# Kernel optimization log

Hardware: AMD Instinct MI355X
Metric: run time of the kernel (lower is better)

Reference implementation:

```python
import jax, jax.numpy as jnp
import numpy as np

N = 50000       # nodes
E = 800000      # edges (before self-loops)
F_IN = 128
HID = 64
HEADS = 4
OUT_DIM = 128
N_CLS = 2
NG = 500        # num graphs
SLOPE = 0.2     # GATConv leaky_relu negative slope
EPS = 1e-5      # BatchNorm eps


def setup_inputs() -> dict:
    key = jax.random.key(0)
    ks = jax.random.split(key, 24)
    s = 0.05
    d = {
        "x": jax.random.normal(ks[0], (N, F_IN), jnp.float32),
        "edge_index": jax.random.randint(ks[1], (2, E), 0, N, jnp.int64),
        "batch": jnp.sort(jax.random.randint(ks[2], (N,), 0, NG, jnp.int64)),
        # GATConv 1
        "W1": jax.random.normal(ks[3], (F_IN, HEADS * HID), jnp.float32) * s,
        "att_src1": jax.random.normal(ks[4], (HEADS, HID), jnp.float32) * s,
        "att_dst1": jax.random.normal(ks[5], (HEADS, HID), jnp.float32) * s,
        "b1": jnp.zeros((HEADS * HID,), jnp.float32),
        # BN1 (eval mode)
        "g1": jnp.ones((HEADS * HID,), jnp.float32),
        "be1": jnp.zeros((HEADS * HID,), jnp.float32),
        "rm1": jnp.zeros((HEADS * HID,), jnp.float32),
        "rv1": jnp.ones((HEADS * HID,), jnp.float32),
        # GATConv 2
        "W2": jax.random.normal(ks[6], (HEADS * HID, HEADS * HID), jnp.float32) * s,
        "att_src2": jax.random.normal(ks[7], (HEADS, HID), jnp.float32) * s,
        "att_dst2": jax.random.normal(ks[8], (HEADS, HID), jnp.float32) * s,
        "b2": jnp.zeros((HEADS * HID,), jnp.float32),
        # BN2 (eval mode)
        "g2": jnp.ones((HEADS * HID,), jnp.float32),
        "be2": jnp.zeros((HEADS * HID,), jnp.float32),
        "rm2": jnp.zeros((HEADS * HID,), jnp.float32),
        "rv2": jnp.ones((HEADS * HID,), jnp.float32),
        # MLP head
        "lw1": jax.random.normal(ks[9], (HEADS * HID, OUT_DIM), jnp.float32) * s,
        "lb1": jnp.zeros((OUT_DIM,), jnp.float32),
        "lw2": jax.random.normal(ks[10], (OUT_DIM, N_CLS), jnp.float32) * s,
        "lb2": jnp.zeros((N_CLS,), jnp.float32),
    }
    return d


def _gat_conv(x, src, dst, W, a_src, a_dst, b):
    """PyG GATConv (concat heads, add_self_loops=True, eval -> no dropout)."""
    n = x.shape[0]
    h = (x @ W).reshape(n, HEADS, -1)            # [N, H, C]
    loop = jnp.arange(n)
    s = jnp.concatenate([src, loop])             # self-loops appended
    d = jnp.concatenate([dst, loop])
    a_s = jnp.sum(h * a_src, axis=-1)            # [N, H]
    a_d = jnp.sum(h * a_dst, axis=-1)            # [N, H]
    e = jax.nn.leaky_relu(a_s[s] + a_d[d], SLOPE)   # [Et, H]
    # softmax over incoming edges per destination node
    m = jax.ops.segment_max(e, d, num_segments=n)
    ex = jnp.exp(e - m[d])
    denom = jax.ops.segment_sum(ex, d, num_segments=n)
    alpha = ex / denom[d]                        # [Et, H]
    msg = h[s] * alpha[:, :, None]               # [Et, H, C]
    out = jax.ops.segment_sum(msg, d, num_segments=n)
    return out.reshape(n, -1) + b


def _bn_eval(x, g, be, rm, rv):
    return (x - rm) * jax.lax.rsqrt(rv + EPS) * g + be


def reference(x, edge_index, batch, W1, att_src1, att_dst1, b1, g1, be1, rm1, rv1,
              W2, att_src2, att_dst2, b2, g2, be2, rm2, rv2, lw1, lb1, lw2, lb2):
    src, dst = edge_index[0], edge_index[1]
    h = jax.nn.relu(_gat_conv(x, src, dst, W1, att_src1, att_dst1, b1))
    h = _bn_eval(h, g1, be1, rm1, rv1)
    h = jax.nn.relu(_gat_conv(h, src, dst, W2, att_src2, att_dst2, b2))
    h = _bn_eval(h, g2, be2, rm2, rv2)
    # global mean pool over graphs
    sums = jax.ops.segment_sum(h, batch, num_segments=NG)
    cnt = jax.ops.segment_sum(jnp.ones((h.shape[0],), h.dtype), batch, num_segments=NG)
    pooled = sums / jnp.clip(cnt, 1.0)[:, None]
    z = jax.nn.relu(pooled @ lw1 + lb1)
    return z @ lw2 + lb2
```

## Files before the change

kernel.cpp:

```cpp
#include <hip/hip_runtime.h>
#include <hip/hip_bf16.h>
#include <math.h>

#define N_NODES 50000
#define M_PAD   50048
#define NBLK_GEMM (M_PAD / 128)
#define N_EDGES 800000
#define F_IN 128
#define HID 64
#define HEADS 4
#define FEAT 256
#define OUT_DIM 128
#define N_CLS 2
#define NG 500
#define SLOPE 0.2f
#define BN_EPS 1e-5f
#define ECAP 64
#define ET (N_EDGES + N_NODES)
#define EH ((ET + 1) / 2)
#define NBLK_BUILD ((EH + 255) / 256)

typedef __attribute__((ext_vector_type(8))) short short8;
typedef __attribute__((ext_vector_type(4))) float floatx4;
typedef __attribute__((ext_vector_type(2))) float floatx2;

__device__ inline unsigned short f2bf(float f) {
    unsigned int u = __float_as_uint(f);
    unsigned int lsb = (u >> 16) & 1u;
    return (unsigned short)((u + 0x7fffu + lsb) >> 16);
}

template<bool AF32, bool BUILD>
__global__ __launch_bounds__(256, 2) void gemm_mfma_gat(
    const void* __restrict__ Av, const unsigned short* __restrict__ BT,
    const float* __restrict__ att_src, const float* __restrict__ att_dst,
    unsigned char* __restrict__ h8, float* __restrict__ a_s,
    float* __restrict__ a_d, int K,
    const int* __restrict__ src, const int* __restrict__ dst,
    int* __restrict__ deg, int* __restrict__ ell,
    int* __restrict__ ovf_cnt, int* __restrict__ ovf) {
    constexpr int LS = 40;
    constexpr int C8 = 272;
    __shared__ __align__(16) unsigned char smem_raw[128 * C8];
    int t = threadIdx.x;

    if (BUILD && blockIdx.x >= NBLK_GEMM) {
        int i = (blockIdx.x - NBLK_GEMM) * 256 + t;
        if (i >= EH) return;
        int ss[2], dd[2], pp[2];
        int nv = 0;
        #pragma unroll
        for (int j = 0; j < 2; j++) {
            int e = i + j * EH;
            if (e < ET) {
                if (e < N_EDGES) { ss[nv] = src[e]; dd[nv] = dst[e]; }
                else             { ss[nv] = dd[nv] = e - N_EDGES; }
                nv++;
            }
        }
        #pragma unroll
        for (int j = 0; j < 2; j++)
            if (j < nv) pp[j] = atomicAdd(&deg[dd[j]], 1);
        #pragma unroll
        for (int j = 0; j < 2; j++) {
            if (j >= nv) continue;
            if (pp[j] < ECAP) {
                ell[dd[j] * ECAP + pp[j]] = ss[j];
            } else {
                int k = atomicAdd(ovf_cnt, 1);
                ovf[2 * k] = ss[j];
                ovf[2 * k + 1] = dd[j];
            }
        }
        return;
    }

    unsigned short* As = (unsigned short*)smem_raw;
    unsigned short* Bs = As + 128 * LS;
    unsigned char*  s8 = smem_raw;
    int lane = t & 63, w = t >> 6;
    int row0 = blockIdx.x * 128;
    int mrow = lane & 15, quad = lane >> 4;

    floatx4 acc[8][4] = {};

    int rA = t >> 2, cA = (t & 3) * 8;

    const unsigned short* Ab = (const unsigned short*)Av;
    const float* Af = (const float*)Av;

    for (int k0 = 0; k0 < K; k0 += 32) {
        #pragma unroll
        for (int j = 0; j < 2; j++) {
            int r = rA + j * 64;
            if (AF32) {
                uint4 pk = make_uint4(0, 0, 0, 0);
                if (row0 + r < N_NODES) {
                    float4 f0 = *(const float4*)&Af[(long long)(row0 + r) * K + k0 + cA];
                    float4 f1 = *(const float4*)&Af[(long long)(row0 + r) * K + k0 + cA + 4];
                    pk.x = (unsigned)f2bf(f0.x) | ((unsigned)f2bf(f0.y) << 16);
                    pk.y = (unsigned)f2bf(f0.z) | ((unsigned)f2bf(f0.w) << 16);
                    pk.z = (unsigned)f2bf(f1.x) | ((unsigned)f2bf(f1.y) << 16);
                    pk.w = (unsigned)f2bf(f1.z) | ((unsigned)f2bf(f1.w) << 16);
                }
                *(uint4*)&As[r * LS + cA] = pk;
            } else {
                *(uint4*)&As[r * LS + cA] = *(const uint4*)&Ab[(long long)(row0 + r) * K + k0 + cA];
            }
        }
        #pragma unroll
        for (int j = 0; j < 4; j++) {
            int r = rA + j * 64;
            *(uint4*)&Bs[r * LS + cA] = *(const uint4*)&BT[(long long)r * K + k0 + cA];
        }
        __syncthreads();
        short8 bf[4];
        #pragma unroll
        for (int ni = 0; ni < 4; ni++)
            bf[ni] = *(const short8*)&Bs[(w * 64 + ni * 16 + mrow) * LS + quad * 8];
        #pragma unroll
        for (int mi = 0; mi < 8; mi++) {
            short8 af = *(const short8*)&As[(mi * 16 + mrow) * LS + quad * 8];
            #pragma unroll
            for (int ni = 0; ni < 4; ni++)
                acc[mi][ni] = __builtin_amdgcn_mfma_f32_16x16x32_bf16(af, bf[ni],
                                                                      acc[mi][ni], 0, 0, 0);
        }
        __syncthreads();
    }

    float ats[4], atd[4];
    #pragma unroll
    for (int ni = 0; ni < 4; ni++) {
        ats[ni] = att_src[w * 64 + ni * 16 + mrow];
        atd[ni] = att_dst[w * 64 + ni * 16 + mrow];
    }
    #pragma unroll
    for (int mi = 0; mi < 8; mi++) {
        #pragma unroll
        for (int r = 0; r < 4; r++) {
            int row = row0 + mi * 16 + quad * 4 + r;
            float ps = 0.f, pd = 0.f;
            #pragma unroll
            for (int ni = 0; ni < 4; ni++) {
                float v = acc[mi][ni][r];
                ps += v * ats[ni];
                pd += v * atd[ni];
            }
            #pragma unroll
            for (int off = 1; off < 16; off <<= 1) {
                ps += __shfl_xor(ps, off);
                pd += __shfl_xor(pd, off);
            }
            if (mrow == 0 && row < N_NODES) {
                a_s[row * 4 + w] = ps;
                a_d[row * 4 + w] = pd;
            }
        }
    }

    #pragma unroll
    for (int mi = 0; mi < 8; mi++)
        #pragma unroll
        for (int r = 0; r < 4; r++) {
            int row = mi * 16 + quad * 4 + r;
            #pragma unroll
            for (int ni = 0; ni < 4; ni += 2) {
                int pk = __builtin_amdgcn_cvt_pk_fp8_f32(acc[mi][ni][r],
                                                         acc[mi][ni + 1][r], 0, false);
                s8[row * C8 + w * 64 + ni * 16 + mrow]       = (unsigned char)(pk & 0xff);
                s8[row * C8 + w * 64 + (ni + 1) * 16 + mrow] = (unsigned char)((pk >> 8) & 0xff);
            }
        }
    __syncthreads();
    {
        int r2 = t >> 1, half = t & 1;
        const uint4* sp = (const uint4*)&s8[r2 * C8 + half * 128];
        uint4* dp = (uint4*)&h8[(long long)(row0 + r2) * FEAT + half * 128];
        #pragma unroll
        for (int k = 0; k < 8; k++)
            dp[k] = sp[k];
    }
}

__global__ void prep(const float* __restrict__ W1, const float* __restrict__ W2,
                     unsigned short* __restrict__ W1T, unsigned short* __restrict__ W2T,
                     int* __restrict__ deg, int* __restrict__ ovf_cnt,
                     unsigned long long* __restrict__ h1bf_pad) {
    int i = blockIdx.x * 256 + threadIdx.x;
    if (i < F_IN * 256) {
        int k = i >> 8, n = i & 255;
        W1T[n * F_IN + k] = f2bf(W1[i]);
    }
    int j = i - F_IN * 256;
    if (j >= 0 && j < FEAT * 256) {
        int k = j >> 8, n = j & 255;
        W2T[n * FEAT + k] = f2bf(W2[j]);
    }
    if (i < N_NODES) deg[i] = 0;
    if (i == 0) *ovf_cnt = 0;
    if (i < (M_PAD - N_NODES) * FEAT / 4) h1bf_pad[i] = 0ULL;
}

__global__ __launch_bounds__(256) void gat_fused(
    const int* __restrict__ deg_arr, const int* __restrict__ ell,
    const int* __restrict__ ovf_cnt, const int* __restrict__ ovf,
    const float* __restrict__ a_s, const float* __restrict__ a_d,
    const unsigned char* __restrict__ h8, const float* __restrict__ bias,
    const float* __restrict__ g, const float* __restrict__ be,
    const float* __restrict__ rm, const float* __restrict__ rv,
    unsigned short* __restrict__ out16) {
    int t = threadIdx.x;
    int lane = t & 63;
    int w = t >> 6;
    int hd = lane >> 4;
    int d = blockIdx.x * 4 + w;

    __shared__ float p_lds[4 * ECAP * 4];
    __shared__ int   o_lds[4 * ECAP];
    float* pw = &p_lds[w * ECAP * 4];
    int*   ow = &o_lds[w * ECAP];

    const unsigned int* __restrict__ H1 = (const unsigned int*)h8;

    int deg = deg_arr[d];
    float4 ad4 = *(const float4*)&a_d[d * 4];

    float den = 0.f;
    float4 acc = make_float4(0.f, 0.f, 0.f, 0.f);

    if (deg <= ECAP) {
        float lg[4] = {-INFINITY, -INFINITY, -INFINITY, -INFINITY};
        if (lane < deg) {
            int s = ell[d * ECAP + lane];
            ow[lane] = s * 64;
            float4 as4 = *(const float4*)&a_s[s * 4];
            float e0 = as4.x + ad4.x; lg[0] = e0 > 0.f ? e0 : SLOPE * e0;
            float e1 = as4.y + ad4.y; lg[1] = e1 > 0.f ? e1 : SLOPE * e1;
            float e2 = as4.z + ad4.z; lg[2] = e2 > 0.f ? e2 : SLOPE * e2;
            float e3 = as4.w + ad4.w; lg[3] = e3 > 0.f ? e3 : SLOPE * e3;
        }
        float mm = fmaxf(fmaxf(lg[0], lg[1]), fmaxf(lg[2], lg[3]));
        #pragma unroll
        for (int off = 1; off < 64; off <<= 1) mm = fmaxf(mm, __shfl_xor(mm, off));
        if (lane < deg) {
            float4 pq;
            pq.x = __expf(lg[0] - mm);
            pq.y = __expf(lg[1] - mm);
            pq.z = __expf(lg[2] - mm);
            pq.w = __expf(lg[3] - mm);
            *(float4*)&pw[lane * 4] = pq;
        }
        int e = 0;
        for (; e + 1 < deg; e += 2) {
            int oA = ow[e], oB = ow[e + 1];
            float pA = pw[e * 4 + hd], pB = pw[(e + 1) * 4 + hd];
            int uA = (int)H1[oA + lane];
            int uB = (int)H1[oB + lane];
            den += pA + pB;
            floatx2 a0 = __builtin_amdgcn_cvt_pk_f32_fp8(uA, false);
            floatx2 a1 = __builtin_amdgcn_cvt_pk_f32_fp8(uA, true);
            floatx2 b0 = __builtin_amdgcn_cvt_pk_f32_fp8(uB, false);
            floatx2 b1 = __builtin_amdgcn_cvt_pk_f32_fp8(uB, true);
            acc.x += pA * a0.x; acc.y += pA * a0.y;
            acc.z += pA * a1.x; acc.w += pA * a1.y;
            acc.x += pB * b0.x; acc.y += pB * b0.y;
            acc.z += pB * b1.x; acc.w += pB * b1.y;
        }
        if (e < deg) {
            int oA = ow[e];
            float pA = pw[e * 4 + hd];
            int uA = (int)H1[oA + lane];
            den += pA;
            floatx2 a0 = __builtin_amdgcn_cvt_pk_f32_fp8(uA, false);
            floatx2 a1 = __builtin_amdgcn_cvt_pk_f32_fp8(uA, true);
            acc.x += pA * a0.x; acc.y += pA * a0.y;
            acc.z += pA * a1.x; acc.w += pA * a1.y;
        }
    } else {
        float m_old;
        {
            int s = ell[d * ECAP + lane];
            ow[lane] = s * 64;
            float4 as4 = *(const float4*)&a_s[s * 4];
            float lg[4];
            float e0 = as4.x + ad4.x; lg[0] = e0 > 0.f ? e0 : SLOPE * e0;
            float e1 = as4.y + ad4.y; lg[1] = e1 > 0.f ? e1 : SLOPE * e1;
            float e2 = as4.z + ad4.z; lg[2] = e2 > 0.f ? e2 : SLOPE * e2;
            float e3 = as4.w + ad4.w; lg[3] = e3 > 0.f ? e3 : SLOPE * e3;
            float mm = fmaxf(fmaxf(lg[0], lg[1]), fmaxf(lg[2], lg[3]));
            #pragma unroll
            for (int off = 1; off < 64; off <<= 1) mm = fmaxf(mm, __shfl_xor(mm, off));
            m_old = mm;
            float4 pq;
            pq.x = __expf(lg[0] - mm);
            pq.y = __expf(lg[1] - mm);
            pq.z = __expf(lg[2] - mm);
            pq.w = __expf(lg[3] - mm);
            *(float4*)&pw[lane * 4] = pq;
            for (int e = 0; e < ECAP; e++) {
                int oA = ow[e];
                float pA = pw[e * 4 + hd];
                int uA = (int)H1[oA + lane];
                den += pA;
                floatx2 a0 = __builtin_amdgcn_cvt_pk_f32_fp8(uA, false);
                floatx2 a1 = __builtin_amdgcn_cvt_pk_f32_fp8(uA, true);
                acc.x += pA * a0.x; acc.y += pA * a0.y;
                acc.z += pA * a1.x; acc.w += pA * a1.y;
            }
        }
        int nov = *ovf_cnt;
        for (int i = 0; i < nov; i++) {
            int s2 = ovf[2 * i], d2 = ovf[2 * i + 1];
            if (d2 != d) continue;
            float4 as4 = *(const float4*)&a_s[s2 * 4];
            float lg[4];
            float e0 = as4.x + ad4.x; lg[0] = e0 > 0.f ? e0 : SLOPE * e0;
            float e1 = as4.y + ad4.y; lg[1] = e1 > 0.f ? e1 : SLOPE * e1;
            float e2 = as4.z + ad4.z; lg[2] = e2 > 0.f ? e2 : SLOPE * e2;
            float e3 = as4.w + ad4.w; lg[3] = e3 > 0.f ? e3 : SLOPE * e3;
            float mmax = fmaxf(fmaxf(lg[0], lg[1]), fmaxf(lg[2], lg[3]));
            float m_new = fmaxf(m_old, mmax);
            float alpha = __expf(m_old - m_new);
            m_old = m_new;
            float ph = __expf(lg[hd] - m_new);
            acc.x *= alpha; acc.y *= alpha; acc.z *= alpha; acc.w *= alpha;
            den = den * alpha + ph;
            int u = (int)H1[s2 * 64 + lane];
            floatx2 a0 = __builtin_amdgcn_cvt_pk_f32_fp8(u, false);
            floatx2 a1 = __builtin_amdgcn_cvt_pk_f32_fp8(u, true);
            acc.x += ph * a0.x; acc.y += ph * a0.y;
            acc.z += ph * a1.x; acc.w += ph * a1.y;
        }
    }
    float inv = 1.f / den;
    int c0 = lane * 4;
    float4 bi = *(const float4*)&bias[c0];
    float4 gg = *(const float4*)&g[c0];
    float4 bb = *(const float4*)&be[c0];
    float4 mm4 = *(const float4*)&rm[c0];
    float4 vv = *(const float4*)&rv[c0];
    float v0 = fmaxf(acc.x * inv + bi.x, 0.f);
    float v1 = fmaxf(acc.y * inv + bi.y, 0.f);
    float v2 = fmaxf(acc.z * inv + bi.z, 0.f);
    float v3 = fmaxf(acc.w * inv + bi.w, 0.f);
    v0 = (v0 - mm4.x) * rsqrtf(vv.x + BN_EPS) * gg.x + bb.x;
    v1 = (v1 - mm4.y) * rsqrtf(vv.y + BN_EPS) * gg.y + bb.y;
    v2 = (v2 - mm4.z) * rsqrtf(vv.z + BN_EPS) * gg.z + bb.z;
    v3 = (v3 - mm4.w) * rsqrtf(vv.w + BN_EPS) * gg.w + bb.w;
    unsigned long long o =
        (unsigned long long)f2bf(v0) |
        ((unsigned long long)f2bf(v1) << 16) |
        ((unsigned long long)f2bf(v2) << 32) |
        ((unsigned long long)f2bf(v3) << 48);
    __builtin_nontemporal_store(o, (unsigned long long*)&out16[(long long)d * FEAT + c0]);
}

__global__ __launch_bounds__(256) void head_fused(
    const unsigned short* __restrict__ h2, const int* __restrict__ batch,
    const float* __restrict__ lw1, const float* __restrict__ lb1,
    const float* __restrict__ lw2, const float* __restrict__ lb2,
    float* __restrict__ out) {
    int gph = blockIdx.x;
    int t = threadIdx.x;
    __shared__ float pooled[FEAT];
    __shared__ float zl[OUT_DIM];
    __shared__ int lo_s, hi_s;
    if (t == 0) {
        int lo = 0, hi = N_NODES;
        while (lo < hi) { int mid = (lo + hi) >> 1; if (batch[mid] < gph) lo = mid + 1; else hi = mid; }
        lo_s = lo;
        int lo2 = 0, hi2 = N_NODES;
        while (lo2 < hi2) { int mid = (lo2 + hi2) >> 1; if (batch[mid] < gph + 1) lo2 = mid + 1; else hi2 = mid; }
        hi_s = lo2;
    }
    __syncthreads();
    int lo = lo_s, hi = hi_s;
    float a0 = 0.f, a1 = 0.f, a2 = 0.f, a3 = 0.f;
    int n = lo;
    for (; n + 3 < hi; n += 4) {
        a0 += __uint_as_float((unsigned)h2[(long long)n * FEAT + t] << 16);
        a1 += __uint_as_float((unsigned)h2[(long long)(n + 1) * FEAT + t] << 16);
        a2 += __uint_as_float((unsigned)h2[(long long)(n + 2) * FEAT + t] << 16);
        a3 += __uint_as_float((unsigned)h2[(long long)(n + 3) * FEAT + t] << 16);
    }
    for (; n < hi; n++) a0 += __uint_as_float((unsigned)h2[(long long)n * FEAT + t] << 16);
    float cnt = fmaxf((float)(hi - lo), 1.f);
    pooled[t] = (a0 + a1 + a2 + a3) / cnt;
    __syncthreads();
    int j = t >> 1, kh = t & 1;
    float zp = 0.f;
    #pragma unroll 8
    for (int k = kh * 128; k < kh * 128 + 128; k++)
        zp += pooled[k] * lw1[k * OUT_DIM + j];
    zp += __shfl_xor(zp, 1);
    if (kh == 0) zl[j] = fmaxf(zp + lb1[j], 0.f);
    __syncthreads();
    int w = t >> 6, lane = t & 63;
    if (w < 2) {
        float p = zl[lane] * lw2[lane * 2 + w] + zl[lane + 64] * lw2[(lane + 64) * 2 + w];
        #pragma unroll
        for (int off = 1; off < 64; off <<= 1) p += __shfl_xor(p, off);
        if (lane == 0) out[gph * 2 + w] = p + lb2[w];
    }
}

extern "C" void kernel_launch(void* const* d_in, const int* in_sizes, int n_in,
                              void* d_out, int out_size, void* d_ws, size_t ws_size,
                              hipStream_t stream) {
    const float* x       = (const float*)d_in[0];
    const int*   ei      = (const int*)d_in[1];
    const int*   batch   = (const int*)d_in[2];
    const float* W1      = (const float*)d_in[3];
    const float* att_s1  = (const float*)d_in[4];
    const float* att_d1  = (const float*)d_in[5];
    const float* b1      = (const float*)d_in[6];
    const float* g1      = (const float*)d_in[7];
    const float* be1     = (const float*)d_in[8];
    const float* rm1     = (const float*)d_in[9];
    const float* rv1     = (const float*)d_in[10];
    const float* W2      = (const float*)d_in[11];
    const float* att_s2  = (const float*)d_in[12];
    const float* att_d2  = (const float*)d_in[13];
    const float* b2      = (const float*)d_in[14];
    const float* g2      = (const float*)d_in[15];
    const float* be2     = (const float*)d_in[16];
    const float* rm2     = (const float*)d_in[17];
    const float* rv2     = (const float*)d_in[18];
    const float* lw1     = (const float*)d_in[19];
    const float* lb1     = (const float*)d_in[20];
    const float* lw2     = (const float*)d_in[21];
    const float* lb2     = (const float*)d_in[22];
    float* out           = (float*)d_out;

    const int* src = ei;
    const int* dst = ei + N_EDGES;

    char* p = (char*)d_ws;
    auto carve = [&p](size_t bytes) -> void* {
        void* r = (void*)p;
        p += (bytes + 63) & ~(size_t)63;
        return r;
    };
    unsigned short* h2bf = (unsigned short*)carve(sizeof(short) * (size_t)N_NODES * FEAT);
    float* a_s    = (float*)carve(sizeof(float) * N_NODES * HEADS);
    float* a_d    = (float*)carve(sizeof(float) * N_NODES * HEADS);
    int*   deg    = (int*)carve(sizeof(int) * N_NODES);
    int*   ell    = (int*)carve(sizeof(int) * (size_t)N_NODES * ECAP);
    int*   ovf_cnt= (int*)carve(sizeof(int) * 16);
    int*   ovf    = (int*)carve(sizeof(int) * 2 * ET);
    unsigned char*  h8   = (unsigned char*)carve((size_t)M_PAD * FEAT);
    unsigned short* h1bf = (unsigned short*)carve(sizeof(short) * (size_t)M_PAD * FEAT);
    unsigned short* w1t  = (unsigned short*)carve(sizeof(short) * FEAT * F_IN);
    unsigned short* w2t  = (unsigned short*)carve(sizeof(short) * FEAT * FEAT);

    prep<<<((F_IN + FEAT) * 256 + 255) / 256, 256, 0, stream>>>(
        W1, W2, w1t, w2t, deg, ovf_cnt,
        (unsigned long long*)(h1bf + (size_t)N_NODES * FEAT));

    gemm_mfma_gat<true, true><<<NBLK_GEMM + NBLK_BUILD, 256, 0, stream>>>(
        x, w1t, att_s1, att_d1, h8, a_s, a_d, F_IN,
        src, dst, deg, ell, ovf_cnt, ovf);
    gat_fused<<<N_NODES / 4, 256, 0, stream>>>(deg, ell, ovf_cnt, ovf, a_s, a_d, h8,
                                               b1, g1, be1, rm1, rv1, h1bf);

    gemm_mfma_gat<false, false><<<NBLK_GEMM, 256, 0, stream>>>(
        h1bf, w2t, att_s2, att_d2, h8, a_s, a_d, FEAT,
        nullptr, nullptr, nullptr, nullptr, nullptr, nullptr);
    gat_fused<<<N_NODES / 4, 256, 0, stream>>>(deg, ell, ovf_cnt, ovf, a_s, a_d, h8,
                                               b2, g2, be2, rm2, rv2, h2bf);

    head_fused<<<NG, 256, 0, stream>>>(h2bf, batch, lw1, lb1, lw2, lb2, out);
}
```

Before: 307.4 us.

## Halve GEMM epilogue LDS and pre-seed self-loops in prep

```diff
diff --git a/kernel.cpp b/kernel.cpp
--- a/kernel.cpp
+++ b/kernel.cpp
@@ -17,8 +17,8 @@
 #define BN_EPS 1e-5f
 #define ECAP 64
 #define ET (N_EDGES + N_NODES)
-#define EH ((ET + 1) / 2)
-#define NBLK_BUILD ((EH + 255) / 256)
+#define EH2 ((N_EDGES + 1) / 2)
+#define NBLK_BUILD ((EH2 + 255) / 256)
 
 typedef __attribute__((ext_vector_type(8))) short short8;
 typedef __attribute__((ext_vector_type(4))) float floatx4;
@@ -41,22 +41,18 @@
     int* __restrict__ ovf_cnt, int* __restrict__ ovf) {
     constexpr int LS = 40;
     constexpr int C8 = 272;
-    __shared__ __align__(16) unsigned char smem_raw[128 * C8];
+    __shared__ __align__(16) unsigned char smem_raw[30720];
     int t = threadIdx.x;
 
     if (BUILD && blockIdx.x >= NBLK_GEMM) {
         int i = (blockIdx.x - NBLK_GEMM) * 256 + t;
-        if (i >= EH) return;
+        if (i >= EH2) return;
         int ss[2], dd[2], pp[2];
         int nv = 0;
         #pragma unroll
         for (int j = 0; j < 2; j++) {
-            int e = i + j * EH;
-            if (e < ET) {
-                if (e < N_EDGES) { ss[nv] = src[e]; dd[nv] = dst[e]; }
-                else             { ss[nv] = dd[nv] = e - N_EDGES; }
-                nv++;
-            }
+            int e = i + j * EH2;
+            if (e < N_EDGES) { ss[nv] = src[e]; dd[nv] = dst[e]; nv++; }
         }
         #pragma unroll
         for (int j = 0; j < 2; j++)
@@ -160,32 +156,35 @@
     }
 
     #pragma unroll
-    for (int mi = 0; mi < 8; mi++)
-        #pragma unroll
-        for (int r = 0; r < 4; r++) {
-            int row = mi * 16 + quad * 4 + r;
+    for (int h = 0; h < 2; h++) {
+        __syncthreads();
+        #pragma unroll
+        for (int mi = h * 4; mi < h * 4 + 4; mi++)
             #pragma unroll
-            for (int ni = 0; ni < 4; ni += 2) {
-                int pk = __builtin_amdgcn_cvt_pk_fp8_f32(acc[mi][ni][r],
-                                                         acc[mi][ni + 1][r], 0, false);
-                s8[row * C8 + w * 64 + ni * 16 + mrow]       = (unsigned char)(pk & 0xff);
-                s8[row * C8 + w * 64 + (ni + 1) * 16 + mrow] = (unsigned char)((pk >> 8) & 0xff);
-            }
-        }
-    __syncthreads();
-    {
-        int r2 = t >> 1, half = t & 1;
-        const uint4* sp = (const uint4*)&s8[r2 * C8 + half * 128];
-        uint4* dp = (uint4*)&h8[(long long)(row0 + r2) * FEAT + half * 128];
-        #pragma unroll
-        for (int k = 0; k < 8; k++)
+            for (int r = 0; r < 4; r++) {
+                int row = (mi - h * 4) * 16 + quad * 4 + r;
+                #pragma unroll
+                for (int ni = 0; ni < 4; ni += 2) {
+                    int pk = __builtin_amdgcn_cvt_pk_fp8_f32(acc[mi][ni][r],
+                                                             acc[mi][ni + 1][r], 0, false);
+                    s8[row * C8 + w * 64 + ni * 16 + mrow]       = (unsigned char)(pk & 0xff);
+                    s8[row * C8 + w * 64 + (ni + 1) * 16 + mrow] = (unsigned char)((pk >> 8) & 0xff);
+                }
+            }
+        __syncthreads();
+        int r2 = t >> 2, q4 = t & 3;
+        const uint4* sp = (const uint4*)&s8[r2 * C8 + q4 * 64];
+        uint4* dp = (uint4*)&h8[(long long)(row0 + h * 64 + r2) * FEAT + q4 * 64];
+        #pragma unroll
+        for (int k = 0; k < 4; k++)
             dp[k] = sp[k];
     }
 }
 
 __global__ void prep(const float* __restrict__ W1, const float* __restrict__ W2,
                      unsigned short* __restrict__ W1T, unsigned short* __restrict__ W2T,
-                     int* __restrict__ deg, int* __restrict__ ovf_cnt,
+                     int* __restrict__ deg, int* __restrict__ ell,
+                     int* __restrict__ ovf_cnt,
                      unsigned long long* __restrict__ h1bf_pad) {
     int i = blockIdx.x * 256 + threadIdx.x;
     if (i < F_IN * 256) {
@@ -197,7 +196,10 @@
         int k = j >> 8, n = j & 255;
         W2T[n * FEAT + k] = f2bf(W2[j]);
     }
-    if (i < N_NODES) deg[i] = 0;
+    if (i < N_NODES) {
+        deg[i] = 1;
+        ell[i * ECAP] = i;
+    }
     if (i == 0) *ovf_cnt = 0;
     if (i < (M_PAD - N_NODES) * FEAT / 4) h1bf_pad[i] = 0ULL;
 }
@@ -455,7 +457,7 @@
     unsigned short* w2t  = (unsigned short*)carve(sizeof(short) * FEAT * FEAT);
 
     prep<<<((F_IN + FEAT) * 256 + 255) / 256, 256, 0, stream>>>(
-        W1, W2, w1t, w2t, deg, ovf_cnt,
+        W1, W2, w1t, w2t, deg, ell, ovf_cnt,
         (unsigned long long*)(h1bf + (size_t)N_NODES * FEAT));
 
     gemm_mfma_gat<true, true><<<NBLK_GEMM + NBLK_BUILD, 256, 0, stream>>>(
```

Measured after the change: 310.4 us. Within noise of the previous version (+0.9%).

## Partition ELL build by destination range and pre-seed self-loops in prep

Applied to the files above, without the earlier changes.

```diff
diff --git a/kernel.cpp b/kernel.cpp
--- a/kernel.cpp
+++ b/kernel.cpp
@@ -17,8 +17,10 @@
 #define BN_EPS 1e-5f
 #define ECAP 64
 #define ET (N_EDGES + N_NODES)
-#define EH ((ET + 1) / 2)
-#define NBLK_BUILD ((EH + 255) / 256)
+#define NCHUNK_B 200
+#define NBLK_BUILD (NCHUNK_B * 8)
+#define CHB ((N_EDGES + NCHUNK_B - 1) / NCHUNK_B)
+#define GS (N_NODES / 8)
 
 typedef __attribute__((ext_vector_type(8))) short short8;
 typedef __attribute__((ext_vector_type(4))) float floatx4;
@@ -45,31 +47,24 @@
     int t = threadIdx.x;
 
     if (BUILD && blockIdx.x >= NBLK_GEMM) {
-        int i = (blockIdx.x - NBLK_GEMM) * 256 + t;
-        if (i >= EH) return;
-        int ss[2], dd[2], pp[2];
-        int nv = 0;
-        #pragma unroll
-        for (int j = 0; j < 2; j++) {
-            int e = i + j * EH;
-            if (e < ET) {
-                if (e < N_EDGES) { ss[nv] = src[e]; dd[nv] = dst[e]; }
-                else             { ss[nv] = dd[nv] = e - N_EDGES; }
-                nv++;
-            }
-        }
-        #pragma unroll
-        for (int j = 0; j < 2; j++)
-            if (j < nv) pp[j] = atomicAdd(&deg[dd[j]], 1);
-        #pragma unroll
-        for (int j = 0; j < 2; j++) {
-            if (j >= nv) continue;
-            if (pp[j] < ECAP) {
-                ell[dd[j] * ECAP + pp[j]] = ss[j];
+        int bi = blockIdx.x - NBLK_GEMM;
+        int g = bi & 7;
+        int chunk = bi >> 3;
+        int lo = chunk * CHB;
+        int hi = min(lo + CHB, N_EDGES);
+        int dlo = g * GS;
+        int dhi = (g == 7) ? N_NODES : dlo + GS;
+        for (int e = lo + t; e < hi; e += 256) {
+            int d = dst[e];
+            if (d < dlo || d >= dhi) continue;
+            int s = src[e];
+            int pos = atomicAdd(&deg[d], 1);
+            if (pos < ECAP) {
+                ell[d * ECAP + pos] = s;
             } else {
                 int k = atomicAdd(ovf_cnt, 1);
-                ovf[2 * k] = ss[j];
-                ovf[2 * k + 1] = dd[j];
+                ovf[2 * k] = s;
+                ovf[2 * k + 1] = d;
             }
         }
         return;
@@ -185,7 +180,8 @@
 
 __global__ void prep(const float* __restrict__ W1, const float* __restrict__ W2,
                      unsigned short* __restrict__ W1T, unsigned short* __restrict__ W2T,
-                     int* __restrict__ deg, int* __restrict__ ovf_cnt,
+                     int* __restrict__ deg, int* __restrict__ ell,
+                     int* __restrict__ ovf_cnt,
                      unsigned long long* __restrict__ h1bf_pad) {
     int i = blockIdx.x * 256 + threadIdx.x;
     if (i < F_IN * 256) {
@@ -197,7 +193,10 @@
         int k = j >> 8, n = j & 255;
         W2T[n * FEAT + k] = f2bf(W2[j]);
     }
-    if (i < N_NODES) deg[i] = 0;
+    if (i < N_NODES) {
+        deg[i] = 1;
+        ell[i * ECAP] = i;
+    }
     if (i == 0) *ovf_cnt = 0;
     if (i < (M_PAD - N_NODES) * FEAT / 4) h1bf_pad[i] = 0ULL;
 }
@@ -455,7 +454,7 @@
     unsigned short* w2t  = (unsigned short*)carve(sizeof(short) * FEAT * FEAT);
 
     prep<<<((F_IN + FEAT) * 256 + 255) / 256, 256, 0, stream>>>(
-        W1, W2, w1t, w2t, deg, ovf_cnt,
+        W1, W2, w1t, w2t, deg, ell, ovf_cnt,
         (unsigned long long*)(h1bf + (size_t)N_NODES * FEAT));
 
     gemm_mfma_gat<true, true><<<NBLK_GEMM + NBLK_BUILD, 256, 0, stream>>>(
```

Result: no change. 308.0 us (+0.2%).
